# Optimization experiments

Hardware: AMD Instinct MI355X
Metric: run time of the kernel (lower is better)

Reference implementation:

```python
import jax, jax.numpy as jnp
import numpy as np


def setup_inputs() -> dict:
    key = jax.random.key(0)
    k1, k2 = jax.random.split(key)
    B, Tq, Tk, D = 8, 2048, 2048, 1024
    query = jax.random.normal(k1, (B, Tq, D), dtype=jnp.float32)
    key_t = jax.random.normal(k2, (B, Tk, D), dtype=jnp.float32)
    return {"query": query, "key": key_t}


def reference(query, key):
    # Unscaled cross attention: key acts as both K and V.
    # energy: [B, Tq, Tk]
    energy = jnp.einsum("bqd,bkd->bqk", query, key)
    attention = jax.nn.softmax(energy, axis=-1)
    # output: [B, Tq, D]
    return jnp.einsum("bqk,bkd->bqd", attention, key)
```

## Files before the change

kernel.cpp:

```cpp
#include <hip/hip_runtime.h>
#include <stdint.h>

typedef int i32x4 __attribute__((ext_vector_type(4)));
typedef int8_t s8;

__device__ __forceinline__ void gload_lds16(const void* g, uint32_t lds_addr) {
  __builtin_amdgcn_global_load_lds(
      (const __attribute__((address_space(1))) void*)(uintptr_t)g,
      (__attribute__((address_space(3))) void*)(uintptr_t)lds_addr,
      16, 0, 0);
}

__device__ __forceinline__ void qsplit(float x, float s, float sinv, float s2inv,
                                       int& q1, int& q2) {
  float a = rintf(x * sinv);
  a = fminf(fmaxf(a, -127.f), 127.f);
  float r = fmaf(a, -s, x);
  float b = fminf(fmaxf(rintf(r * s2inv), -127.f), 127.f);
  q1 = (int)a; q2 = (int)b;
}
__device__ __forceinline__ uint32_t pack4(int b0, int b1, int b2, int b3) {
  return ((uint32_t)(uint8_t)b0) | ((uint32_t)(uint8_t)b1 << 8) |
         ((uint32_t)(uint8_t)b2 << 16) | ((uint32_t)(uint8_t)b3 << 24);
}

#define SQ (8.0f / 127.0f)
#define SQ_INV 15.875f
#define SQ2_INV 2032.0f

__global__ __launch_bounds__(256) void cvt_q_i8(const float* __restrict__ x,
                                                s8* __restrict__ a, s8* __restrict__ b) {
  size_t i = ((size_t)blockIdx.x * 256 + threadIdx.x) * 8;
  float4 v0 = ((const float4*)(x + i))[0];
  float4 v1 = ((const float4*)(x + i))[1];
  float f[8] = {v0.x, v0.y, v0.z, v0.w, v1.x, v1.y, v1.z, v1.w};
  int q1[8], q2[8];
#pragma unroll
  for (int j = 0; j < 8; j++) qsplit(f[j], SQ, SQ_INV, SQ2_INV, q1[j], q2[j]);
  uint2 ua, ub;
  ua.x = pack4(q1[0], q1[1], q1[2], q1[3]); ua.y = pack4(q1[4], q1[5], q1[6], q1[7]);
  ub.x = pack4(q2[0], q2[1], q2[2], q2[3]); ub.y = pack4(q2[4], q2[5], q2[6], q2[7]);
  *(uint2*)(a + i) = ua;
  *(uint2*)(b + i) = ub;
}

__global__ __launch_bounds__(256) void cvt_k_i8(const float* __restrict__ K,
                                                s8* __restrict__ k1, s8* __restrict__ k2,
                                                s8* __restrict__ t1, s8* __restrict__ t2) {
  __shared__ uint32_t tile[64][33];
  const int b = blockIdx.z;
  const int d0 = blockIdx.x * 32, t0 = blockIdx.y * 64;
  const int tid = threadIdx.x;
  const float* Kb = K + (size_t)b * 2048 * 1024;
  {
    const int t = tid >> 2, d8 = (tid & 3) * 8;
    const float* src = Kb + (size_t)(t0 + t) * 1024 + d0 + d8;
    float4 v0 = ((const float4*)src)[0];
    float4 v1 = ((const float4*)src)[1];
    float f[8] = {v0.x, v0.y, v0.z, v0.w, v1.x, v1.y, v1.z, v1.w};
    int q1[8], q2[8];
#pragma unroll
    for (int j = 0; j < 8; j++) {
      qsplit(f[j], SQ, SQ_INV, SQ2_INV, q1[j], q2[j]);
      tile[t][d8 + j] = ((uint32_t)(uint8_t)q1[j]) | ((uint32_t)(uint8_t)q2[j] << 8);
    }
    uint2 ua, ub;
    ua.x = pack4(q1[0], q1[1], q1[2], q1[3]); ua.y = pack4(q1[4], q1[5], q1[6], q1[7]);
    ub.x = pack4(q2[0], q2[1], q2[2], q2[3]); ub.y = pack4(q2[4], q2[5], q2[6], q2[7]);
    size_t off = (size_t)b * 2048 * 1024 + (size_t)(t0 + t) * 1024 + d0 + d8;
    *(uint2*)(k1 + off) = ua;
    *(uint2*)(k2 + off) = ub;
  }
  __syncthreads();
  {
    const int d = tid >> 3, tg = tid & 7;
    uint32_t v[8];
#pragma unroll
    for (int i = 0; i < 8; i++) v[i] = tile[tg * 8 + i][d];
    uint2 ua, ub;
    ua.x = pack4(v[0], v[1], v[2], v[3]); ua.y = pack4(v[4], v[5], v[6], v[7]);
    ub.x = pack4(v[0] >> 8, v[1] >> 8, v[2] >> 8, v[3] >> 8);
    ub.y = pack4(v[4] >> 8, v[5] >> 8, v[6] >> 8, v[7] >> 8);
    size_t off = (size_t)b * 1024 * 2048 + (size_t)(d0 + d) * 2048 + t0 + tg * 8;
    *(uint2*)(t1 + off) = ua;
    *(uint2*)(t2 + off) = ub;
  }
}

__global__ __launch_bounds__(256) void softmax_i8(const float* __restrict__ E,
                                                  s8* __restrict__ P1, s8* __restrict__ P2) {
  const size_t row = blockIdx.x;
  const float* e = E + row * 2048;
  const int t = threadIdx.x;
  float4 a = ((const float4*)e)[t * 2];
  float4 b = ((const float4*)e)[t * 2 + 1];
  float f[8] = {a.x, a.y, a.z, a.w, b.x, b.y, b.z, b.w};
  float m = f[0];
#pragma unroll
  for (int j = 1; j < 8; j++) m = fmaxf(m, f[j]);
#pragma unroll
  for (int off = 32; off > 0; off >>= 1) m = fmaxf(m, __shfl_down(m, off));
  __shared__ float redm[4], reds[4];
  if ((t & 63) == 0) redm[t >> 6] = m;
  __syncthreads();
  m = fmaxf(fmaxf(redm[0], redm[1]), fmaxf(redm[2], redm[3]));
  float ex[8];
  float s = 0.f;
#pragma unroll
  for (int j = 0; j < 8; j++) { ex[j] = __expf(f[j] - m); s += ex[j]; }
#pragma unroll
  for (int off = 32; off > 0; off >>= 1) s += __shfl_down(s, off);
  if ((t & 63) == 0) reds[t >> 6] = s;
  __syncthreads();
  s = reds[0] + reds[1] + reds[2] + reds[3];
  float inv = 1.0f / s;
  int q1[8], q2[8];
#pragma unroll
  for (int j = 0; j < 8; j++)
    qsplit(ex[j] * inv, 1.0f / 127.0f, 127.0f, 16256.0f, q1[j], q2[j]);
  uint2 ua, ub;
  ua.x = pack4(q1[0], q1[1], q1[2], q1[3]); ua.y = pack4(q1[4], q1[5], q1[6], q1[7]);
  ub.x = pack4(q2[0], q2[1], q2[2], q2[3]); ub.y = pack4(q2[4], q2[5], q2[6], q2[7]);
  *(uint2*)(P1 + row * 2048 + t * 8) = ua;
  *(uint2*)(P2 + row * 2048 + t * 8) = ub;
}

__global__ __launch_bounds__(256) void gemm1_i8(
    const s8* __restrict__ A0, const s8* __restrict__ A1,
    const s8* __restrict__ B0, const s8* __restrict__ B1,
    float* __restrict__ C, int Kdim, int ldc, long sA, long sB, long sC) {
  __shared__ char lds[2][32768];
  const int tid = threadIdx.x;
  const int w = tid >> 6, l = tid & 63;
  const int bz = blockIdx.z;
  const int rowA = blockIdx.y * 128, rowB = blockIdx.x * 128;
  const s8* bases[4] = {A0 + bz * sA, A1 + bz * sA, B0 + bz * sB, B1 + bz * sB};
  const int rbase[4] = {rowA, rowA, rowB, rowB};
  const s8* gp[8];
  uint32_t lpo[8];
#pragma unroll
  for (int i = 0; i < 8; i++) {
    int gc = w * 8 + i;
    int buf = gc >> 3, c = gc & 7;
    int row = c * 16 + (l >> 2);
    int q = (l & 3) ^ ((row >> 1) & 3);
    gp[i] = bases[buf] + (size_t)(rbase[buf] + row) * Kdim + q * 16;
    lpo[i] = (uint32_t)(uintptr_t)(&lds[0][0] + buf * 8192 + c * 1024 + l * 16);
  }
  i32x4 acc1[4][4], acc2[4][4];
  const i32x4 zero = {0, 0, 0, 0};
#pragma unroll
  for (int mt = 0; mt < 4; mt++)
#pragma unroll
    for (int nt = 0; nt < 4; nt++) { acc1[mt][nt] = zero; acc2[mt][nt] = zero; }

  const int wm = w & 1, wn = w >> 1, q4 = l >> 4, rl = l & 15;

#pragma unroll
  for (int i = 0; i < 8; i++) { gload_lds16(gp[i], lpo[i]); gp[i] += 64; }
  __syncthreads();

  int cur = 0;
  for (int k0 = 0; k0 < Kdim; k0 += 64) {
    if (k0 + 64 < Kdim) {
      const uint32_t nb = (uint32_t)(cur ^ 1) * 32768u;
#pragma unroll
      for (int i = 0; i < 8; i++) { gload_lds16(gp[i], lpo[i] + nb); gp[i] += 64; }
    }
    const char* L = &lds[cur][0];
    i32x4 af[2][4], bfr[2][4];
#pragma unroll
    for (int mt = 0; mt < 4; mt++) {
      int row = wm * 64 + mt * 16 + rl;
      int off = row * 64 + ((q4 ^ ((row >> 1) & 3)) << 4);
      af[0][mt] = *(const i32x4*)(L + off);
      af[1][mt] = *(const i32x4*)(L + 8192 + off);
    }
#pragma unroll
    for (int nt = 0; nt < 4; nt++) {
      int row = wn * 64 + nt * 16 + rl;
      int off = row * 64 + ((q4 ^ ((row >> 1) & 3)) << 4);
      bfr[0][nt] = *(const i32x4*)(L + 16384 + off);
      bfr[1][nt] = *(const i32x4*)(L + 24576 + off);
    }
#pragma unroll
    for (int mt = 0; mt < 4; mt++)
#pragma unroll
      for (int nt = 0; nt < 4; nt++) {
        acc1[mt][nt] = __builtin_amdgcn_mfma_i32_16x16x64_i8(af[0][mt], bfr[0][nt], acc1[mt][nt], 0, 0, 0);
        acc2[mt][nt] = __builtin_amdgcn_mfma_i32_16x16x64_i8(af[0][mt], bfr[1][nt], acc2[mt][nt], 0, 0, 0);
        acc2[mt][nt] = __builtin_amdgcn_mfma_i32_16x16x64_i8(af[1][mt], bfr[0][nt], acc2[mt][nt], 0, 0, 0);
      }
    __syncthreads();
    cur ^= 1;
  }
  const float c1 = 64.0f / 16129.0f, c2 = c1 * (1.0f / 128.0f);
  float* Cb = C + (size_t)bz * sC + (size_t)rowA * ldc + rowB;
#pragma unroll
  for (int mt = 0; mt < 4; mt++)
#pragma unroll
    for (int nt = 0; nt < 4; nt++)
#pragma unroll
      for (int r = 0; r < 4; r++)
        Cb[(size_t)(wm * 64 + mt * 16 + q4 * 4 + r) * ldc + (wn * 64 + nt * 16 + rl)] =
            c1 * (float)acc1[mt][nt][r] + c2 * (float)acc2[mt][nt][r];
}

__global__ __launch_bounds__(256) void gemm2_i8(
    const s8* __restrict__ A0, const s8* __restrict__ A1,
    const s8* __restrict__ B0, const s8* __restrict__ B1,
    float* __restrict__ C, int Kdim, int ldc, long sA, long sB, long sC) {
  __shared__ char lds[2][24576];
  const int tid = threadIdx.x;
  const int w = tid >> 6, l = tid & 63;
  const int bz = blockIdx.z;
  const int rowA = blockIdx.y * 128, rowB = blockIdx.x * 64;
  const s8* bases[4] = {A0 + bz * sA, A1 + bz * sA, B0 + bz * sB, B1 + bz * sB};
  const int rbase[4] = {rowA, rowA, rowB, rowB};
  const int bufoff[4] = {0, 8192, 16384, 20480};
  const s8* gp[6];
  uint32_t lpo[6];
#pragma unroll
  for (int i = 0; i < 6; i++) {
    int gc = w * 6 + i;
    int buf, c;
    if (gc < 8) { buf = 0; c = gc; }
    else if (gc < 16) { buf = 1; c = gc - 8; }
    else if (gc < 20) { buf = 2; c = gc - 16; }
    else { buf = 3; c = gc - 20; }
    int row = c * 16 + (l >> 2);
    int q = (l & 3) ^ ((row >> 1) & 3);
    gp[i] = bases[buf] + (size_t)(rbase[buf] + row) * Kdim + q * 16;
    lpo[i] = (uint32_t)(uintptr_t)(&lds[0][0] + bufoff[buf] + c * 1024 + l * 16);
  }
  i32x4 acc1[4][2], acc2[4][2];
  const i32x4 zero = {0, 0, 0, 0};
#pragma unroll
  for (int mt = 0; mt < 4; mt++)
#pragma unroll
    for (int nt = 0; nt < 2; nt++) { acc1[mt][nt] = zero; acc2[mt][nt] = zero; }

  const int wm = w & 1, wn = w >> 1, q4 = l >> 4, rl = l & 15;

#pragma unroll
  for (int i = 0; i < 6; i++) { gload_lds16(gp[i], lpo[i]); gp[i] += 64; }
  __syncthreads();

  int cur = 0;
  for (int k0 = 0; k0 < Kdim; k0 += 64) {
    if (k0 + 64 < Kdim) {
      const uint32_t nb = (uint32_t)(cur ^ 1) * 24576u;
#pragma unroll
      for (int i = 0; i < 6; i++) { gload_lds16(gp[i], lpo[i] + nb); gp[i] += 64; }
    }
    const char* L = &lds[cur][0];
    i32x4 af[2][4], bfr[2][2];
#pragma unroll
    for (int mt = 0; mt < 4; mt++) {
      int row = wm * 64 + mt * 16 + rl;
      int off = row * 64 + ((q4 ^ ((row >> 1) & 3)) << 4);
      af[0][mt] = *(const i32x4*)(L + off);
      af[1][mt] = *(const i32x4*)(L + 8192 + off);
    }
#pragma unroll
    for (int nt = 0; nt < 2; nt++) {
      int row = wn * 32 + nt * 16 + rl;
      int off = row * 64 + ((q4 ^ ((row >> 1) & 3)) << 4);
      bfr[0][nt] = *(const i32x4*)(L + 16384 + off);
      bfr[1][nt] = *(const i32x4*)(L + 20480 + off);
    }
#pragma unroll
    for (int mt = 0; mt < 4; mt++)
#pragma unroll
      for (int nt = 0; nt < 2; nt++) {
        acc1[mt][nt] = __builtin_amdgcn_mfma_i32_16x16x64_i8(af[0][mt], bfr[0][nt], acc1[mt][nt], 0, 0, 0);
        acc2[mt][nt] = __builtin_amdgcn_mfma_i32_16x16x64_i8(af[0][mt], bfr[1][nt], acc2[mt][nt], 0, 0, 0);
        acc2[mt][nt] = __builtin_amdgcn_mfma_i32_16x16x64_i8(af[1][mt], bfr[0][nt], acc2[mt][nt], 0, 0, 0);
      }
    __syncthreads();
    cur ^= 1;
  }
  const float c1 = 8.0f / 16129.0f, c2 = c1 * (1.0f / 128.0f);
  float* Cb = C + (size_t)bz * sC + (size_t)rowA * ldc + rowB;
#pragma unroll
  for (int mt = 0; mt < 4; mt++)
#pragma unroll
    for (int nt = 0; nt < 2; nt++)
#pragma unroll
      for (int r = 0; r < 4; r++)
        Cb[(size_t)(wm * 64 + mt * 16 + q4 * 4 + r) * ldc + (wn * 32 + nt * 16 + rl)] =
            c1 * (float)acc1[mt][nt][r] + c2 * (float)acc2[mt][nt][r];
}

extern "C" void kernel_launch(void* const* d_in, const int* in_sizes, int n_in,
                              void* d_out, int out_size, void* d_ws, size_t ws_size,
                              hipStream_t stream) {
  (void)in_sizes; (void)n_in; (void)out_size;
  const float* Q = (const float*)d_in[0];
  const float* K = (const float*)d_in[1];
  float* O = (float*)d_out;
  const int Btot = 8, Tq = 2048, Tk = 2048, D = 1024;
  const size_t perb = 36ull << 20;
  int NB = 8;
  while (NB > 1 && (size_t)NB * perb > ws_size) NB >>= 1;

  char* p = (char*)d_ws;
  const size_t qd = (size_t)NB * Tq * D;
  const size_t kd = (size_t)NB * Tk * D;
  const size_t ee = (size_t)NB * Tq * Tk;
  s8* Q1 = (s8*)p; p += qd;
  s8* Q2 = (s8*)p; p += qd;
  s8* K1 = (s8*)p; p += kd;
  s8* K2 = (s8*)p; p += kd;
  s8* KT1 = (s8*)p; p += kd;
  s8* KT2 = (s8*)p; p += kd;
  float* E = (float*)p; p += ee * 4;
  s8* P1 = (s8*)p; p += ee;
  s8* P2 = (s8*)p; p += ee;

  for (int c = 0; c < Btot / NB; c++) {
    const float* Qc = Q + (size_t)c * qd;
    const float* Kc = K + (size_t)c * kd;
    float* Oc = O + (size_t)c * qd;
    cvt_q_i8<<<dim3(NB * 1024), 256, 0, stream>>>(Qc, Q1, Q2);
    cvt_k_i8<<<dim3(32, 32, NB), 256, 0, stream>>>(Kc, K1, K2, KT1, KT2);
    gemm1_i8<<<dim3(16, 16, NB), 256, 0, stream>>>(
        Q1, Q2, K1, K2, E, 1024, 2048, (long)Tq * D, (long)Tk * D, (long)Tq * Tk);
    softmax_i8<<<dim3(NB * Tq), 256, 0, stream>>>(E, P1, P2);
    gemm2_i8<<<dim3(16, 16, NB), 256, 0, stream>>>(
        P1, P2, KT1, KT2, Oc, 2048, 1024, (long)Tq * Tk, (long)D * Tk, (long)Tq * D);
  }
}
```

Baseline: 478.4 us.

## Use 8 waves per block in int8 GEMMs with explicit vmcnt waits and barriers

Both int8 split-precision GEMMs now launch 512 threads per block instead of 256. The wave tile is halved (wave grid 2x4) and each thread issues fewer global-to-LDS loads. The __syncthreads double-buffer pattern is replaced by raw s_barrier plus s_waitcnt vmcnt, so the prefetch of the next tile stays in flight while the current one is consumed. The aim is more waves to hide latency and lower register pressure per wave, at the cost of less fragment reuse per wave and more LDS read traffic.

```diff
diff --git a/kernel.cpp b/kernel.cpp
--- a/kernel.cpp
+++ b/kernel.cpp
@@ -125,7 +125,7 @@
   *(uint2*)(P2 + row * 2048 + t * 8) = ub;
 }
 
-__global__ __launch_bounds__(256) void gemm1_i8(
+__global__ __launch_bounds__(512, 2) void gemm1_i8(
     const s8* __restrict__ A0, const s8* __restrict__ A1,
     const s8* __restrict__ B0, const s8* __restrict__ B1,
     float* __restrict__ C, int Kdim, int ldc, long sA, long sB, long sC) {
@@ -136,39 +136,44 @@
   const int rowA = blockIdx.y * 128, rowB = blockIdx.x * 128;
   const s8* bases[4] = {A0 + bz * sA, A1 + bz * sA, B0 + bz * sB, B1 + bz * sB};
   const int rbase[4] = {rowA, rowA, rowB, rowB};
-  const s8* gp[8];
-  uint32_t lpo[8];
-#pragma unroll
-  for (int i = 0; i < 8; i++) {
-    int gc = w * 8 + i;
+  const s8* gp[4];
+  uint32_t lpo[4];
+#pragma unroll
+  for (int i = 0; i < 4; i++) {
+    int gc = w * 4 + i;
     int buf = gc >> 3, c = gc & 7;
     int row = c * 16 + (l >> 2);
     int q = (l & 3) ^ ((row >> 1) & 3);
     gp[i] = bases[buf] + (size_t)(rbase[buf] + row) * Kdim + q * 16;
     lpo[i] = (uint32_t)(uintptr_t)(&lds[0][0] + buf * 8192 + c * 1024 + l * 16);
   }
-  i32x4 acc1[4][4], acc2[4][4];
+  i32x4 acc1[4][2], acc2[4][2];
   const i32x4 zero = {0, 0, 0, 0};
 #pragma unroll
   for (int mt = 0; mt < 4; mt++)
 #pragma unroll
-    for (int nt = 0; nt < 4; nt++) { acc1[mt][nt] = zero; acc2[mt][nt] = zero; }
-
-  const int wm = w & 1, wn = w >> 1, q4 = l >> 4, rl = l & 15;
-
-#pragma unroll
-  for (int i = 0; i < 8; i++) { gload_lds16(gp[i], lpo[i]); gp[i] += 64; }
-  __syncthreads();
+    for (int nt = 0; nt < 2; nt++) { acc1[mt][nt] = zero; acc2[mt][nt] = zero; }
+
+  const int wm = w >> 2, wn = w & 3, q4 = l >> 4, rl = l & 15;
+
+#pragma unroll
+  for (int i = 0; i < 4; i++) { gload_lds16(gp[i], lpo[i]); gp[i] += 64; }
 
   int cur = 0;
   for (int k0 = 0; k0 < Kdim; k0 += 64) {
+    __builtin_amdgcn_s_barrier();
     if (k0 + 64 < Kdim) {
       const uint32_t nb = (uint32_t)(cur ^ 1) * 32768u;
 #pragma unroll
-      for (int i = 0; i < 8; i++) { gload_lds16(gp[i], lpo[i] + nb); gp[i] += 64; }
-    }
+      for (int i = 0; i < 4; i++) { gload_lds16(gp[i], lpo[i] + nb); gp[i] += 64; }
+      asm volatile("s_waitcnt vmcnt(4)" ::: "memory");
+    } else {
+      asm volatile("s_waitcnt vmcnt(0)" ::: "memory");
+    }
+    __builtin_amdgcn_sched_barrier(0);
+    __builtin_amdgcn_s_barrier();
     const char* L = &lds[cur][0];
-    i32x4 af[2][4], bfr[2][4];
+    i32x4 af[2][4], bfr[2][2];
 #pragma unroll
     for (int mt = 0; mt < 4; mt++) {
       int row = wm * 64 + mt * 16 + rl;
@@ -177,8 +182,8 @@
       af[1][mt] = *(const i32x4*)(L + 8192 + off);
     }
 #pragma unroll
-    for (int nt = 0; nt < 4; nt++) {
-      int row = wn * 64 + nt * 16 + rl;
+    for (int nt = 0; nt < 2; nt++) {
+      int row = wn * 32 + nt * 16 + rl;
       int off = row * 64 + ((q4 ^ ((row >> 1) & 3)) << 4);
       bfr[0][nt] = *(const i32x4*)(L + 16384 + off);
       bfr[1][nt] = *(const i32x4*)(L + 24576 + off);
@@ -186,12 +191,11 @@
 #pragma unroll
     for (int mt = 0; mt < 4; mt++)
 #pragma unroll
-      for (int nt = 0; nt < 4; nt++) {
+      for (int nt = 0; nt < 2; nt++) {
         acc1[mt][nt] = __builtin_amdgcn_mfma_i32_16x16x64_i8(af[0][mt], bfr[0][nt], acc1[mt][nt], 0, 0, 0);
         acc2[mt][nt] = __builtin_amdgcn_mfma_i32_16x16x64_i8(af[0][mt], bfr[1][nt], acc2[mt][nt], 0, 0, 0);
         acc2[mt][nt] = __builtin_amdgcn_mfma_i32_16x16x64_i8(af[1][mt], bfr[0][nt], acc2[mt][nt], 0, 0, 0);
       }
-    __syncthreads();
     cur ^= 1;
   }
   const float c1 = 64.0f / 16129.0f, c2 = c1 * (1.0f / 128.0f);
@@ -199,14 +203,14 @@
 #pragma unroll
   for (int mt = 0; mt < 4; mt++)
 #pragma unroll
-    for (int nt = 0; nt < 4; nt++)
+    for (int nt = 0; nt < 2; nt++)
 #pragma unroll
       for (int r = 0; r < 4; r++)
-        Cb[(size_t)(wm * 64 + mt * 16 + q4 * 4 + r) * ldc + (wn * 64 + nt * 16 + rl)] =
+        Cb[(size_t)(wm * 64 + mt * 16 + q4 * 4 + r) * ldc + (wn * 32 + nt * 16 + rl)] =
             c1 * (float)acc1[mt][nt][r] + c2 * (float)acc2[mt][nt][r];
 }
 
-__global__ __launch_bounds__(256) void gemm2_i8(
+__global__ __launch_bounds__(512, 2) void gemm2_i8(
     const s8* __restrict__ A0, const s8* __restrict__ A1,
     const s8* __restrict__ B0, const s8* __restrict__ B1,
     float* __restrict__ C, int Kdim, int ldc, long sA, long sB, long sC) {
@@ -218,11 +222,11 @@
   const s8* bases[4] = {A0 + bz * sA, A1 + bz * sA, B0 + bz * sB, B1 + bz * sB};
   const int rbase[4] = {rowA, rowA, rowB, rowB};
   const int bufoff[4] = {0, 8192, 16384, 20480};
-  const s8* gp[6];
-  uint32_t lpo[6];
-#pragma unroll
-  for (int i = 0; i < 6; i++) {
-    int gc = w * 6 + i;
+  const s8* gp[3];
+  uint32_t lpo[3];
+#pragma unroll
+  for (int i = 0; i < 3; i++) {
+    int gc = w * 3 + i;
     int buf, c;
     if (gc < 8) { buf = 0; c = gc; }
     else if (gc < 16) { buf = 1; c = gc - 8; }
@@ -233,28 +237,31 @@
     gp[i] = bases[buf] + (size_t)(rbase[buf] + row) * Kdim + q * 16;
     lpo[i] = (uint32_t)(uintptr_t)(&lds[0][0] + bufoff[buf] + c * 1024 + l * 16);
   }
-  i32x4 acc1[4][2], acc2[4][2];
+  i32x4 acc1[4], acc2[4];
   const i32x4 zero = {0, 0, 0, 0};
 #pragma unroll
-  for (int mt = 0; mt < 4; mt++)
-#pragma unroll
-    for (int nt = 0; nt < 2; nt++) { acc1[mt][nt] = zero; acc2[mt][nt] = zero; }
-
-  const int wm = w & 1, wn = w >> 1, q4 = l >> 4, rl = l & 15;
-
-#pragma unroll
-  for (int i = 0; i < 6; i++) { gload_lds16(gp[i], lpo[i]); gp[i] += 64; }
-  __syncthreads();
+  for (int mt = 0; mt < 4; mt++) { acc1[mt] = zero; acc2[mt] = zero; }
+
+  const int wm = w >> 2, wn = w & 3, q4 = l >> 4, rl = l & 15;
+
+#pragma unroll
+  for (int i = 0; i < 3; i++) { gload_lds16(gp[i], lpo[i]); gp[i] += 64; }
 
   int cur = 0;
   for (int k0 = 0; k0 < Kdim; k0 += 64) {
+    __builtin_amdgcn_s_barrier();
     if (k0 + 64 < Kdim) {
       const uint32_t nb = (uint32_t)(cur ^ 1) * 24576u;
 #pragma unroll
-      for (int i = 0; i < 6; i++) { gload_lds16(gp[i], lpo[i] + nb); gp[i] += 64; }
-    }
+      for (int i = 0; i < 3; i++) { gload_lds16(gp[i], lpo[i] + nb); gp[i] += 64; }
+      asm volatile("s_waitcnt vmcnt(3)" ::: "memory");
+    } else {
+      asm volatile("s_waitcnt vmcnt(0)" ::: "memory");
+    }
+    __builtin_amdgcn_sched_barrier(0);
+    __builtin_amdgcn_s_barrier();
     const char* L = &lds[cur][0];
-    i32x4 af[2][4], bfr[2][2];
+    i32x4 af[2][4], bf0, bf1;
 #pragma unroll
     for (int mt = 0; mt < 4; mt++) {
       int row = wm * 64 + mt * 16 + rl;
@@ -262,22 +269,18 @@
       af[0][mt] = *(const i32x4*)(L + off);
       af[1][mt] = *(const i32x4*)(L + 8192 + off);
     }
-#pragma unroll
-    for (int nt = 0; nt < 2; nt++) {
-      int row = wn * 32 + nt * 16 + rl;
+    {
+      int row = wn * 16 + rl;
       int off = row * 64 + ((q4 ^ ((row >> 1) & 3)) << 4);
-      bfr[0][nt] = *(const i32x4*)(L + 16384 + off);
-      bfr[1][nt] = *(const i32x4*)(L + 20480 + off);
-    }
-#pragma unroll
-    for (int mt = 0; mt < 4; mt++)
-#pragma unroll
-      for (int nt = 0; nt < 2; nt++) {
-        acc1[mt][nt] = __builtin_amdgcn_mfma_i32_16x16x64_i8(af[0][mt], bfr[0][nt], acc1[mt][nt], 0, 0, 0);
-        acc2[mt][nt] = __builtin_amdgcn_mfma_i32_16x16x64_i8(af[0][mt], bfr[1][nt], acc2[mt][nt], 0, 0, 0);
-        acc2[mt][nt] = __builtin_amdgcn_mfma_i32_16x16x64_i8(af[1][mt], bfr[0][nt], acc2[mt][nt], 0, 0, 0);
-      }
-    __syncthreads();
+      bf0 = *(const i32x4*)(L + 16384 + off);
+      bf1 = *(const i32x4*)(L + 20480 + off);
+    }
+#pragma unroll
+    for (int mt = 0; mt < 4; mt++) {
+      acc1[mt] = __builtin_amdgcn_mfma_i32_16x16x64_i8(af[0][mt], bf0, acc1[mt], 0, 0, 0);
+      acc2[mt] = __builtin_amdgcn_mfma_i32_16x16x64_i8(af[0][mt], bf1, acc2[mt], 0, 0, 0);
+      acc2[mt] = __builtin_amdgcn_mfma_i32_16x16x64_i8(af[1][mt], bf0, acc2[mt], 0, 0, 0);
+    }
     cur ^= 1;
   }
   const float c1 = 8.0f / 16129.0f, c2 = c1 * (1.0f / 128.0f);
@@ -285,11 +288,9 @@
 #pragma unroll
   for (int mt = 0; mt < 4; mt++)
 #pragma unroll
-    for (int nt = 0; nt < 2; nt++)
-#pragma unroll
-      for (int r = 0; r < 4; r++)
-        Cb[(size_t)(wm * 64 + mt * 16 + q4 * 4 + r) * ldc + (wn * 32 + nt * 16 + rl)] =
-            c1 * (float)acc1[mt][nt][r] + c2 * (float)acc2[mt][nt][r];
+    for (int r = 0; r < 4; r++)
+      Cb[(size_t)(wm * 64 + mt * 16 + q4 * 4 + r) * ldc + (wn * 16 + rl)] =
+          c1 * (float)acc1[mt][r] + c2 * (float)acc2[mt][r];
 }
 
 extern "C" void kernel_launch(void* const* d_in, const int* in_sizes, int n_in,
@@ -324,10 +325,10 @@
     float* Oc = O + (size_t)c * qd;
     cvt_q_i8<<<dim3(NB * 1024), 256, 0, stream>>>(Qc, Q1, Q2);
     cvt_k_i8<<<dim3(32, 32, NB), 256, 0, stream>>>(Kc, K1, K2, KT1, KT2);
-    gemm1_i8<<<dim3(16, 16, NB), 256, 0, stream>>>(
+    gemm1_i8<<<dim3(16, 16, NB), 512, 0, stream>>>(
         Q1, Q2, K1, K2, E, 1024, 2048, (long)Tq * D, (long)Tk * D, (long)Tq * Tk);
     softmax_i8<<<dim3(NB * Tq), 256, 0, stream>>>(E, P1, P2);
-    gemm2_i8<<<dim3(16, 16, NB), 256, 0, stream>>>(
+    gemm2_i8<<<dim3(16, 16, NB), 512, 0, stream>>>(
         P1, P2, KT1, KT2, Oc, 2048, 1024, (long)Tq * Tk, (long)D * Tk, (long)Tq * D);
   }
 }
```

Measured after the change: 435.5 us. 9.0% less time.

## Unify int8 GEMMs with 128x128 tiles and finer-grained vmcnt barrier pipeline

Applied to the files above, without the earlier changes.

Replaces the separate gemm2 kernel (128x64 tiles) with the shared 128x128-tile kernel, so the second GEMM runs half as many blocks but each block gets more reuse. The K-loop swaps the __syncthreads pair for raw s_barrier plus an explicit s_waitcnt vmcnt(8), so the prefetch for the next stage stays in flight while the current tile is consumed. B fragments are now loaded per column tile and interleaved with the MFMAs to cut register pressure, with launch_bounds(256,2) to target two blocks per CU. Risks: the hand-written barrier and waitcnt logic may race on LDS, and the larger tiles reduce the block count for gemm2.

```diff
diff --git a/kernel.cpp b/kernel.cpp
--- a/kernel.cpp
+++ b/kernel.cpp
@@ -125,10 +125,11 @@
   *(uint2*)(P2 + row * 2048 + t * 8) = ub;
 }
 
-__global__ __launch_bounds__(256) void gemm1_i8(
+__global__ __launch_bounds__(256, 2) void gemm_i8(
     const s8* __restrict__ A0, const s8* __restrict__ A1,
     const s8* __restrict__ B0, const s8* __restrict__ B1,
-    float* __restrict__ C, int Kdim, int ldc, long sA, long sB, long sC) {
+    float* __restrict__ C, int Kdim, int ldc, long sA, long sB, long sC,
+    float c1, float c2) {
   __shared__ char lds[2][32768];
   const int tid = threadIdx.x;
   const int w = tid >> 6, l = tid & 63;
@@ -158,43 +159,44 @@
 
 #pragma unroll
   for (int i = 0; i < 8; i++) { gload_lds16(gp[i], lpo[i]); gp[i] += 64; }
-  __syncthreads();
 
   int cur = 0;
   for (int k0 = 0; k0 < Kdim; k0 += 64) {
+    __builtin_amdgcn_s_barrier();
     if (k0 + 64 < Kdim) {
       const uint32_t nb = (uint32_t)(cur ^ 1) * 32768u;
 #pragma unroll
       for (int i = 0; i < 8; i++) { gload_lds16(gp[i], lpo[i] + nb); gp[i] += 64; }
-    }
+      asm volatile("s_waitcnt vmcnt(8)" ::: "memory");
+    } else {
+      asm volatile("s_waitcnt vmcnt(0)" ::: "memory");
+    }
+    __builtin_amdgcn_sched_barrier(0);
+    __builtin_amdgcn_s_barrier();
     const char* L = &lds[cur][0];
-    i32x4 af[2][4], bfr[2][4];
+    i32x4 af0[4], af1[4];
 #pragma unroll
     for (int mt = 0; mt < 4; mt++) {
       int row = wm * 64 + mt * 16 + rl;
       int off = row * 64 + ((q4 ^ ((row >> 1) & 3)) << 4);
-      af[0][mt] = *(const i32x4*)(L + off);
-      af[1][mt] = *(const i32x4*)(L + 8192 + off);
+      af0[mt] = *(const i32x4*)(L + off);
+      af1[mt] = *(const i32x4*)(L + 8192 + off);
     }
 #pragma unroll
     for (int nt = 0; nt < 4; nt++) {
       int row = wn * 64 + nt * 16 + rl;
       int off = row * 64 + ((q4 ^ ((row >> 1) & 3)) << 4);
-      bfr[0][nt] = *(const i32x4*)(L + 16384 + off);
-      bfr[1][nt] = *(const i32x4*)(L + 24576 + off);
-    }
-#pragma unroll
-    for (int mt = 0; mt < 4; mt++)
-#pragma unroll
-      for (int nt = 0; nt < 4; nt++) {
-        acc1[mt][nt] = __builtin_amdgcn_mfma_i32_16x16x64_i8(af[0][mt], bfr[0][nt], acc1[mt][nt], 0, 0, 0);
-        acc2[mt][nt] = __builtin_amdgcn_mfma_i32_16x16x64_i8(af[0][mt], bfr[1][nt], acc2[mt][nt], 0, 0, 0);
-        acc2[mt][nt] = __builtin_amdgcn_mfma_i32_16x16x64_i8(af[1][mt], bfr[0][nt], acc2[mt][nt], 0, 0, 0);
+      i32x4 bf0 = *(const i32x4*)(L + 16384 + off);
+      i32x4 bf1 = *(const i32x4*)(L + 24576 + off);
+#pragma unroll
+      for (int mt = 0; mt < 4; mt++) {
+        acc1[mt][nt] = __builtin_amdgcn_mfma_i32_16x16x64_i8(af0[mt], bf0, acc1[mt][nt], 0, 0, 0);
+        acc2[mt][nt] = __builtin_amdgcn_mfma_i32_16x16x64_i8(af0[mt], bf1, acc2[mt][nt], 0, 0, 0);
+        acc2[mt][nt] = __builtin_amdgcn_mfma_i32_16x16x64_i8(af1[mt], bf0, acc2[mt][nt], 0, 0, 0);
       }
-    __syncthreads();
+    }
     cur ^= 1;
   }
-  const float c1 = 64.0f / 16129.0f, c2 = c1 * (1.0f / 128.0f);
   float* Cb = C + (size_t)bz * sC + (size_t)rowA * ldc + rowB;
 #pragma unroll
   for (int mt = 0; mt < 4; mt++)
@@ -203,92 +205,6 @@
 #pragma unroll
       for (int r = 0; r < 4; r++)
         Cb[(size_t)(wm * 64 + mt * 16 + q4 * 4 + r) * ldc + (wn * 64 + nt * 16 + rl)] =
-            c1 * (float)acc1[mt][nt][r] + c2 * (float)acc2[mt][nt][r];
-}
-
-__global__ __launch_bounds__(256) void gemm2_i8(
-    const s8* __restrict__ A0, const s8* __restrict__ A1,
-    const s8* __restrict__ B0, const s8* __restrict__ B1,
-    float* __restrict__ C, int Kdim, int ldc, long sA, long sB, long sC) {
-  __shared__ char lds[2][24576];
-  const int tid = threadIdx.x;
-  const int w = tid >> 6, l = tid & 63;
-  const int bz = blockIdx.z;
-  const int rowA = blockIdx.y * 128, rowB = blockIdx.x * 64;
-  const s8* bases[4] = {A0 + bz * sA, A1 + bz * sA, B0 + bz * sB, B1 + bz * sB};
-  const int rbase[4] = {rowA, rowA, rowB, rowB};
-  const int bufoff[4] = {0, 8192, 16384, 20480};
-  const s8* gp[6];
-  uint32_t lpo[6];
-#pragma unroll
-  for (int i = 0; i < 6; i++) {
-    int gc = w * 6 + i;
-    int buf, c;
-    if (gc < 8) { buf = 0; c = gc; }
-    else if (gc < 16) { buf = 1; c = gc - 8; }
-    else if (gc < 20) { buf = 2; c = gc - 16; }
-    else { buf = 3; c = gc - 20; }
-    int row = c * 16 + (l >> 2);
-    int q = (l & 3) ^ ((row >> 1) & 3);
-    gp[i] = bases[buf] + (size_t)(rbase[buf] + row) * Kdim + q * 16;
-    lpo[i] = (uint32_t)(uintptr_t)(&lds[0][0] + bufoff[buf] + c * 1024 + l * 16);
-  }
-  i32x4 acc1[4][2], acc2[4][2];
-  const i32x4 zero = {0, 0, 0, 0};
-#pragma unroll
-  for (int mt = 0; mt < 4; mt++)
-#pragma unroll
-    for (int nt = 0; nt < 2; nt++) { acc1[mt][nt] = zero; acc2[mt][nt] = zero; }
-
-  const int wm = w & 1, wn = w >> 1, q4 = l >> 4, rl = l & 15;
-
-#pragma unroll
-  for (int i = 0; i < 6; i++) { gload_lds16(gp[i], lpo[i]); gp[i] += 64; }
-  __syncthreads();
-
-  int cur = 0;
-  for (int k0 = 0; k0 < Kdim; k0 += 64) {
-    if (k0 + 64 < Kdim) {
-      const uint32_t nb = (uint32_t)(cur ^ 1) * 24576u;
-#pragma unroll
-      for (int i = 0; i < 6; i++) { gload_lds16(gp[i], lpo[i] + nb); gp[i] += 64; }
-    }
-    const char* L = &lds[cur][0];
-    i32x4 af[2][4], bfr[2][2];
-#pragma unroll
-    for (int mt = 0; mt < 4; mt++) {
-      int row = wm * 64 + mt * 16 + rl;
-      int off = row * 64 + ((q4 ^ ((row >> 1) & 3)) << 4);
-      af[0][mt] = *(const i32x4*)(L + off);
-      af[1][mt] = *(const i32x4*)(L + 8192 + off);
-    }
-#pragma unroll
-    for (int nt = 0; nt < 2; nt++) {
-      int row = wn * 32 + nt * 16 + rl;
-      int off = row * 64 + ((q4 ^ ((row >> 1) & 3)) << 4);
-      bfr[0][nt] = *(const i32x4*)(L + 16384 + off);
-      bfr[1][nt] = *(const i32x4*)(L + 20480 + off);
-    }
-#pragma unroll
-    for (int mt = 0; mt < 4; mt++)
-#pragma unroll
-      for (int nt = 0; nt < 2; nt++) {
-        acc1[mt][nt] = __builtin_amdgcn_mfma_i32_16x16x64_i8(af[0][mt], bfr[0][nt], acc1[mt][nt], 0, 0, 0);
-        acc2[mt][nt] = __builtin_amdgcn_mfma_i32_16x16x64_i8(af[0][mt], bfr[1][nt], acc2[mt][nt], 0, 0, 0);
-        acc2[mt][nt] = __builtin_amdgcn_mfma_i32_16x16x64_i8(af[1][mt], bfr[0][nt], acc2[mt][nt], 0, 0, 0);
-      }
-    __syncthreads();
-    cur ^= 1;
-  }
-  const float c1 = 8.0f / 16129.0f, c2 = c1 * (1.0f / 128.0f);
-  float* Cb = C + (size_t)bz * sC + (size_t)rowA * ldc + rowB;
-#pragma unroll
-  for (int mt = 0; mt < 4; mt++)
-#pragma unroll
-    for (int nt = 0; nt < 2; nt++)
-#pragma unroll
-      for (int r = 0; r < 4; r++)
-        Cb[(size_t)(wm * 64 + mt * 16 + q4 * 4 + r) * ldc + (wn * 32 + nt * 16 + rl)] =
             c1 * (float)acc1[mt][nt][r] + c2 * (float)acc2[mt][nt][r];
 }
 
@@ -318,16 +234,21 @@
   s8* P1 = (s8*)p; p += ee;
   s8* P2 = (s8*)p; p += ee;
 
+  const float g1c1 = 64.0f / 16129.0f, g1c2 = g1c1 * (1.0f / 128.0f);
+  const float g2c1 = 8.0f / 16129.0f, g2c2 = g2c1 * (1.0f / 128.0f);
+
   for (int c = 0; c < Btot / NB; c++) {
     const float* Qc = Q + (size_t)c * qd;
     const float* Kc = K + (size_t)c * kd;
     float* Oc = O + (size_t)c * qd;
     cvt_q_i8<<<dim3(NB * 1024), 256, 0, stream>>>(Qc, Q1, Q2);
     cvt_k_i8<<<dim3(32, 32, NB), 256, 0, stream>>>(Kc, K1, K2, KT1, KT2);
-    gemm1_i8<<<dim3(16, 16, NB), 256, 0, stream>>>(
-        Q1, Q2, K1, K2, E, 1024, 2048, (long)Tq * D, (long)Tk * D, (long)Tq * Tk);
+    gemm_i8<<<dim3(16, 16, NB), 256, 0, stream>>>(
+        Q1, Q2, K1, K2, E, 1024, 2048, (long)Tq * D, (long)Tk * D, (long)Tq * Tk,
+        g1c1, g1c2);
     softmax_i8<<<dim3(NB * Tq), 256, 0, stream>>>(E, P1, P2);
-    gemm2_i8<<<dim3(16, 16, NB), 256, 0, stream>>>(
-        P1, P2, KT1, KT2, Oc, 2048, 1024, (long)Tq * Tk, (long)D * Tk, (long)Tq * D);
-  }
-}
+    gemm_i8<<<dim3(8, 16, NB), 256, 0, stream>>>(
+        P1, P2, KT1, KT2, Oc, 2048, 1024, (long)Tq * Tk, (long)D * Tk, (long)Tq * D,
+        g2c1, g2c2);
+  }
+}
```

After: 427.0 us. 1.12x faster.
